# Kernel optimization log

Measured on AMD Instinct MI355X. Metric: run time of the kernel, lower is better.

## Reference

```python
import jax, jax.numpy as jnp
import numpy as np

T = 2048  # number of simulation steps


def setup_inputs() -> dict:
    key = jax.random.key(0)
    ks = jax.random.split(key, 7)
    B = 8192
    X = jax.random.uniform(ks[0], (T, B), dtype=jnp.float32)
    w_beta = jax.random.uniform(ks[1], (B,), dtype=jnp.float32)
    w_gamma = jax.random.uniform(ks[2], (B,), dtype=jnp.float32)
    w_sigma = jax.random.uniform(ks[3], (B,), dtype=jnp.float32)
    S0 = jax.random.uniform(ks[4], (B,), dtype=jnp.float32)
    I0 = jax.random.uniform(ks[5], (B,), dtype=jnp.float32)
    R0 = jax.random.uniform(ks[6], (B,), dtype=jnp.float32)
    N = jnp.ones((B,), dtype=jnp.float32)
    return {"X": X, "w_beta": w_beta, "w_gamma": w_gamma, "w_sigma": w_sigma,
            "S0": S0, "I0": I0, "R0": R0, "N": N}


def reference(X, w_beta, w_gamma, w_sigma, S0, I0, R0, N):
    # SEIR recurrence: state vectors of size B, scanned over T-1 steps.
    E0 = jnp.zeros_like(S0)

    def step(carry, x_t):
        S, E, I, R = carry
        beta = x_t * w_beta
        gamma = x_t * w_gamma
        sigma = x_t * w_sigma
        S_to_E = beta * I * S / N
        E_to_I = sigma * E
        I_to_R = gamma * I
        Sn = S - S_to_E
        En = E + S_to_E - E_to_I
        In = I + E_to_I - I_to_R
        Rn = R + I_to_R
        return (Sn, En, In, Rn), (Sn, En, In, Rn)

    # original loop runs t = 0 .. T-2, using X[t] at each step
    (_, _, _, _), (Ss, Es, Is, Rs) = jax.lax.scan(
        step, (S0, E0, I0, R0), X[: T - 1])

    S_ = jnp.concatenate([S0[None], Ss], axis=0)  # [T, B]
    E_ = jnp.concatenate([E0[None], Es], axis=0)
    I_ = jnp.concatenate([I0[None], Is], axis=0)
    R_ = jnp.concatenate([R0[None], Rs], axis=0)
    return S_, E_, I_, R_
```

## Files before the change

kernel.cpp:

```cpp
#include <hip/hip_runtime.h>

#define TSTEPS 2048
#define BCOLS  8192
#define TBSZ   (TSTEPS * BCOLS)
#define CHUNKS 32
#define CLEN   64

__device__ __forceinline__ void seir_step(float x, float wb, float wg, float wsg,
                                          float invN,
                                          float& S, float& E, float& I, float& R)
{
    const float s2e = x * wb * I * S * invN;
    const float e2i = x * wsg * E;
    const float i2r = x * wg * I;
    S = S - s2e;
    E = E + s2e - e2i;
    I = I + e2i - i2r;
    R = R + i2r;
}

__global__ __launch_bounds__(64)
void seir_pass1(const float* __restrict__ X,
                const float* __restrict__ w_beta,
                const float* __restrict__ w_gamma,
                const float* __restrict__ w_sigma,
                const float* __restrict__ S0,
                const float* __restrict__ I0,
                const float* __restrict__ R0,
                const float* __restrict__ Nv,
                float* __restrict__ wsp)
{
    const int b = blockIdx.x * 64 + threadIdx.x;

    const float wb  = w_beta[b];
    const float wg  = w_gamma[b];
    const float wsg = w_sigma[b];
    float S = S0[b];
    float E = 0.0f;
    float I = I0[b];
    float R = R0[b];
    const float invN = 1.0f / Nv[b];

    const float* xp = X + b;
    float xbuf[48];
#pragma unroll
    for (int k = 0; k < 48; ++k)
        xbuf[k] = xp[(size_t)k * BCOLS];
    xp += (size_t)48 * BCOLS;

    for (int j = 0; j < 41; ++j) {
        const int tbase = j * 48;
#pragma unroll
        for (int k = 0; k < 48; ++k) {
            const float x = xbuf[k];
            xbuf[k] = xp[(size_t)k * BCOLS];
            seir_step(x, wb, wg, wsg, invN, S, E, I, R);
            const int t = tbase + k;
            if (((t - 62) & 63) == 0) {
                const int idx = (t - 62) >> 6;
                float* wp = wsp + (size_t)idx * 4 * BCOLS + b;
                wp[0]                  = S;
                wp[(size_t)BCOLS]      = E;
                wp[(size_t)2 * BCOLS]  = I;
                wp[(size_t)3 * BCOLS]  = R;
            }
        }
        xp += (size_t)48 * BCOLS;
    }
#pragma unroll
    for (int k = 0; k < 15; ++k) {
        const float x = xbuf[k];
        seir_step(x, wb, wg, wsg, invN, S, E, I, R);
        if (((1968 + k - 62) & 63) == 0) {
            const int idx = (1968 + k - 62) >> 6;
            float* wp = wsp + (size_t)idx * 4 * BCOLS + b;
            wp[0]                  = S;
            wp[(size_t)BCOLS]      = E;
            wp[(size_t)2 * BCOLS]  = I;
            wp[(size_t)3 * BCOLS]  = R;
        }
    }
}

template <int NS>
__device__ __forceinline__ void run_chunk(const float* __restrict__ xp,
                                          float* __restrict__ pS,
                                          float* __restrict__ pE,
                                          float* __restrict__ pI,
                                          float* __restrict__ pR,
                                          float wb, float wg, float wsg, float invN,
                                          float S, float E, float I, float R)
{
    float xbuf[8];
#pragma unroll
    for (int k = 0; k < 8; ++k)
        xbuf[k] = xp[(size_t)k * BCOLS];
#pragma unroll
    for (int t = 0; t < NS; ++t) {
        const float x = xbuf[t & 7];
        if (t + 8 < NS)
            xbuf[t & 7] = xp[(size_t)(t + 8) * BCOLS];
        seir_step(x, wb, wg, wsg, invN, S, E, I, R);
        __builtin_nontemporal_store(S, pS + (size_t)t * BCOLS);
        __builtin_nontemporal_store(E, pE + (size_t)t * BCOLS);
        __builtin_nontemporal_store(I, pI + (size_t)t * BCOLS);
        __builtin_nontemporal_store(R, pR + (size_t)t * BCOLS);
    }
}

__global__ __launch_bounds__(64)
void seir_pass2(const float* __restrict__ X,
                const float* __restrict__ w_beta,
                const float* __restrict__ w_gamma,
                const float* __restrict__ w_sigma,
                const float* __restrict__ S0,
                const float* __restrict__ I0,
                const float* __restrict__ R0,
                const float* __restrict__ Nv,
                const float* __restrict__ wsp,
                float* __restrict__ out)
{
    const int b = blockIdx.x * 64 + threadIdx.x;
    const int c = blockIdx.y;

    const float wb  = w_beta[b];
    const float wg  = w_gamma[b];
    const float wsg = w_sigma[b];
    const float invN = 1.0f / Nv[b];

    float* oS = out + b;
    float* oE = out + (size_t)TBSZ + b;
    float* oI = out + (size_t)2 * TBSZ + b;
    float* oR = out + (size_t)3 * TBSZ + b;

    if (c == 0) {
        float S = S0[b];
        float E = 0.0f;
        float I = I0[b];
        float R = R0[b];
        __builtin_nontemporal_store(S, oS);
        __builtin_nontemporal_store(0.0f, oE);
        __builtin_nontemporal_store(I, oI);
        __builtin_nontemporal_store(R, oR);
        run_chunk<63>(X + b,
                      oS + BCOLS, oE + BCOLS, oI + BCOLS, oR + BCOLS,
                      wb, wg, wsg, invN, S, E, I, R);
    } else {
        const float* wp = wsp + (size_t)(c - 1) * 4 * BCOLS + b;
        const float S = wp[0];
        const float E = wp[(size_t)BCOLS];
        const float I = wp[(size_t)2 * BCOLS];
        const float R = wp[(size_t)3 * BCOLS];
        const size_t t0 = (size_t)c * CLEN - 1;
        const size_t r0 = (size_t)c * CLEN;
        run_chunk<64>(X + t0 * BCOLS + b,
                      oS + r0 * BCOLS, oE + r0 * BCOLS,
                      oI + r0 * BCOLS, oR + r0 * BCOLS,
                      wb, wg, wsg, invN, S, E, I, R);
    }
}

__global__ __launch_bounds__(64)
void seir_mono(const float* __restrict__ X,
               const float* __restrict__ w_beta,
               const float* __restrict__ w_gamma,
               const float* __restrict__ w_sigma,
               const float* __restrict__ S0,
               const float* __restrict__ I0,
               const float* __restrict__ R0,
               const float* __restrict__ Nv,
               float* __restrict__ out)
{
    const int b = blockIdx.x * 64 + threadIdx.x;
    const float wb  = w_beta[b];
    const float wg  = w_gamma[b];
    const float wsg = w_sigma[b];
    float S = S0[b];
    float E = 0.0f;
    float I = I0[b];
    float R = R0[b];
    const float invN = 1.0f / Nv[b];

    float* oS = out + b;
    float* oE = out + (size_t)TBSZ + b;
    float* oI = out + (size_t)2 * TBSZ + b;
    float* oR = out + (size_t)3 * TBSZ + b;

    __builtin_nontemporal_store(S, oS);
    __builtin_nontemporal_store(0.0f, oE);
    __builtin_nontemporal_store(I, oI);
    __builtin_nontemporal_store(R, oR);

    const float* xp = X + b;
    float xc[8];
#pragma unroll
    for (int k = 0; k < 8; ++k)
        xc[k] = __builtin_nontemporal_load(xp + (size_t)k * BCOLS);
    xp += (size_t)8 * BCOLS;

    for (int i = 0; i < 255; ++i) {
        float xn[8];
#pragma unroll
        for (int k = 0; k < 8; ++k)
            xn[k] = __builtin_nontemporal_load(xp + (size_t)k * BCOLS);
        xp += (size_t)8 * BCOLS;

        float* pS = oS + (size_t)(8 * i + 1) * BCOLS;
        float* pE = oE + (size_t)(8 * i + 1) * BCOLS;
        float* pI = oI + (size_t)(8 * i + 1) * BCOLS;
        float* pR = oR + (size_t)(8 * i + 1) * BCOLS;

#pragma unroll
        for (int k = 0; k < 8; ++k) {
            seir_step(xc[k], wb, wg, wsg, invN, S, E, I, R);
            __builtin_nontemporal_store(S, pS + (size_t)k * BCOLS);
            __builtin_nontemporal_store(E, pE + (size_t)k * BCOLS);
            __builtin_nontemporal_store(I, pI + (size_t)k * BCOLS);
            __builtin_nontemporal_store(R, pR + (size_t)k * BCOLS);
        }
#pragma unroll
        for (int k = 0; k < 8; ++k) xc[k] = xn[k];
    }
    {
        float* pS = oS + (size_t)2041 * BCOLS;
        float* pE = oE + (size_t)2041 * BCOLS;
        float* pI = oI + (size_t)2041 * BCOLS;
        float* pR = oR + (size_t)2041 * BCOLS;
#pragma unroll
        for (int k = 0; k < 7; ++k) {
            seir_step(xc[k], wb, wg, wsg, invN, S, E, I, R);
            __builtin_nontemporal_store(S, pS + (size_t)k * BCOLS);
            __builtin_nontemporal_store(E, pE + (size_t)k * BCOLS);
            __builtin_nontemporal_store(I, pI + (size_t)k * BCOLS);
            __builtin_nontemporal_store(R, pR + (size_t)k * BCOLS);
        }
    }
}

extern "C" void kernel_launch(void* const* d_in, const int* in_sizes, int n_in,
                              void* d_out, int out_size, void* d_ws, size_t ws_size,
                              hipStream_t stream)
{
    const float* X      = (const float*)d_in[0];
    const float* w_beta = (const float*)d_in[1];
    const float* w_gamma= (const float*)d_in[2];
    const float* w_sigma= (const float*)d_in[3];
    const float* S0     = (const float*)d_in[4];
    const float* I0     = (const float*)d_in[5];
    const float* R0     = (const float*)d_in[6];
    const float* Nv     = (const float*)d_in[7];
    float* out          = (float*)d_out;

    const size_t need = (size_t)(CHUNKS - 1) * 4 * BCOLS * sizeof(float);
    if (ws_size < need) {
        seir_mono<<<dim3(BCOLS / 64), dim3(64), 0, stream>>>(
            X, w_beta, w_gamma, w_sigma, S0, I0, R0, Nv, out);
        return;
    }

    float* wsp = (float*)d_ws;
    seir_pass1<<<dim3(BCOLS / 64), dim3(64), 0, stream>>>(
        X, w_beta, w_gamma, w_sigma, S0, I0, R0, Nv, wsp);
    seir_pass2<<<dim3(BCOLS / 64, CHUNKS), dim3(64), 0, stream>>>(
        X, w_beta, w_gamma, w_sigma, S0, I0, R0, Nv, wsp, out);
}
```

Before: 378.1 us.

## Fuse checkpoint and chunk-replay passes into one persistent kernel with flag handoff

Replaces the two-kernel scheme (a serial checkpoint pass, then a chunked replay that writes the output) with a single launch. Producer blocks run the full recurrence at raised priority and publish per-chunk state checkpoints with release flags. Consumer blocks spin on those flags and replay their chunks, so output writing overlaps the serial scan instead of waiting for it to finish. The change adds a memset, spin-waits that depend on producers and consumers being co-resident, and a timeout fallback that recomputes the prefix from scratch.

Result: slower. 1.315 ms (+247.7%).

```diff
diff --git a/kernel.cpp b/kernel.cpp
--- a/kernel.cpp
+++ b/kernel.cpp
@@ -5,6 +5,10 @@
 #define TBSZ   (TSTEPS * BCOLS)
 #define CHUNKS 32
 #define CLEN   64
+#define NGRP   128
+#define PBLK   32
+#define NCONS  512
+#define RING   32
 
 __device__ __forceinline__ void seir_step(float x, float wb, float wg, float wsg,
                                           float invN,
@@ -17,69 +21,6 @@
     E = E + s2e - e2i;
     I = I + e2i - i2r;
     R = R + i2r;
-}
-
-__global__ __launch_bounds__(64)
-void seir_pass1(const float* __restrict__ X,
-                const float* __restrict__ w_beta,
-                const float* __restrict__ w_gamma,
-                const float* __restrict__ w_sigma,
-                const float* __restrict__ S0,
-                const float* __restrict__ I0,
-                const float* __restrict__ R0,
-                const float* __restrict__ Nv,
-                float* __restrict__ wsp)
-{
-    const int b = blockIdx.x * 64 + threadIdx.x;
-
-    const float wb  = w_beta[b];
-    const float wg  = w_gamma[b];
-    const float wsg = w_sigma[b];
-    float S = S0[b];
-    float E = 0.0f;
-    float I = I0[b];
-    float R = R0[b];
-    const float invN = 1.0f / Nv[b];
-
-    const float* xp = X + b;
-    float xbuf[48];
-#pragma unroll
-    for (int k = 0; k < 48; ++k)
-        xbuf[k] = xp[(size_t)k * BCOLS];
-    xp += (size_t)48 * BCOLS;
-
-    for (int j = 0; j < 41; ++j) {
-        const int tbase = j * 48;
-#pragma unroll
-        for (int k = 0; k < 48; ++k) {
-            const float x = xbuf[k];
-            xbuf[k] = xp[(size_t)k * BCOLS];
-            seir_step(x, wb, wg, wsg, invN, S, E, I, R);
-            const int t = tbase + k;
-            if (((t - 62) & 63) == 0) {
-                const int idx = (t - 62) >> 6;
-                float* wp = wsp + (size_t)idx * 4 * BCOLS + b;
-                wp[0]                  = S;
-                wp[(size_t)BCOLS]      = E;
-                wp[(size_t)2 * BCOLS]  = I;
-                wp[(size_t)3 * BCOLS]  = R;
-            }
-        }
-        xp += (size_t)48 * BCOLS;
-    }
-#pragma unroll
-    for (int k = 0; k < 15; ++k) {
-        const float x = xbuf[k];
-        seir_step(x, wb, wg, wsg, invN, S, E, I, R);
-        if (((1968 + k - 62) & 63) == 0) {
-            const int idx = (1968 + k - 62) >> 6;
-            float* wp = wsp + (size_t)idx * 4 * BCOLS + b;
-            wp[0]                  = S;
-            wp[(size_t)BCOLS]      = E;
-            wp[(size_t)2 * BCOLS]  = I;
-            wp[(size_t)3 * BCOLS]  = R;
-        }
-    }
 }
 
 template <int NS>
@@ -108,26 +49,15 @@
     }
 }
 
-__global__ __launch_bounds__(64)
-void seir_pass2(const float* __restrict__ X,
-                const float* __restrict__ w_beta,
-                const float* __restrict__ w_gamma,
-                const float* __restrict__ w_sigma,
-                const float* __restrict__ S0,
-                const float* __restrict__ I0,
-                const float* __restrict__ R0,
-                const float* __restrict__ Nv,
-                const float* __restrict__ wsp,
-                float* __restrict__ out)
-{
-    const int b = blockIdx.x * 64 + threadIdx.x;
-    const int c = blockIdx.y;
-
-    const float wb  = w_beta[b];
-    const float wg  = w_gamma[b];
-    const float wsg = w_sigma[b];
-    const float invN = 1.0f / Nv[b];
-
+__device__ __forceinline__ void consume_chunk(
+    int c, int b, int g,
+    const float* __restrict__ X,
+    const float* __restrict__ S0, const float* __restrict__ I0,
+    const float* __restrict__ R0,
+    const float* __restrict__ wsp, const unsigned* __restrict__ flags,
+    float* __restrict__ out,
+    float wb, float wg, float wsg, float invN)
+{
     float* oS = out + b;
     float* oE = out + (size_t)TBSZ + b;
     float* oI = out + (size_t)2 * TBSZ + b;
@@ -145,18 +75,133 @@
         run_chunk<63>(X + b,
                       oS + BCOLS, oE + BCOLS, oI + BCOLS, oR + BCOLS,
                       wb, wg, wsg, invN, S, E, I, R);
+        return;
+    }
+
+    const unsigned* fp = &flags[(c - 1) * NGRP + g];
+    unsigned f;
+    int spins = 0;
+    while ((f = __hip_atomic_load(fp, __ATOMIC_ACQUIRE,
+                                  __HIP_MEMORY_SCOPE_AGENT)) == 0u) {
+        __builtin_amdgcn_s_sleep(8);
+        if (++spins > (1 << 20)) break;
+    }
+
+    float S, E, I, R;
+    if (f != 0u) {
+        const float* wp = wsp + (size_t)(c - 1) * 4 * BCOLS + b;
+        S = wp[0];
+        E = wp[(size_t)BCOLS];
+        I = wp[(size_t)2 * BCOLS];
+        R = wp[(size_t)3 * BCOLS];
     } else {
-        const float* wp = wsp + (size_t)(c - 1) * 4 * BCOLS + b;
-        const float S = wp[0];
-        const float E = wp[(size_t)BCOLS];
-        const float I = wp[(size_t)2 * BCOLS];
-        const float R = wp[(size_t)3 * BCOLS];
-        const size_t t0 = (size_t)c * CLEN - 1;
-        const size_t r0 = (size_t)c * CLEN;
-        run_chunk<64>(X + t0 * BCOLS + b,
-                      oS + r0 * BCOLS, oE + r0 * BCOLS,
-                      oI + r0 * BCOLS, oR + r0 * BCOLS,
-                      wb, wg, wsg, invN, S, E, I, R);
+        S = S0[b];
+        E = 0.0f;
+        I = I0[b];
+        R = R0[b];
+        const float* xq = X + b;
+        const int nst = 64 * c - 1;
+#pragma unroll 4
+        for (int t = 0; t < nst; ++t)
+            seir_step(xq[(size_t)t * BCOLS], wb, wg, wsg, invN, S, E, I, R);
+    }
+
+    const size_t t0 = (size_t)c * CLEN - 1;
+    const size_t r0 = (size_t)c * CLEN;
+    run_chunk<64>(X + t0 * BCOLS + b,
+                  oS + r0 * BCOLS, oE + r0 * BCOLS,
+                  oI + r0 * BCOLS, oR + r0 * BCOLS,
+                  wb, wg, wsg, invN, S, E, I, R);
+}
+
+__global__ __launch_bounds__(256, 4)
+void seir_fused(const float* __restrict__ X,
+                const float* __restrict__ w_beta,
+                const float* __restrict__ w_gamma,
+                const float* __restrict__ w_sigma,
+                const float* __restrict__ S0,
+                const float* __restrict__ I0,
+                const float* __restrict__ R0,
+                const float* __restrict__ Nv,
+                float* __restrict__ wsp,
+                unsigned* __restrict__ flags,
+                float* __restrict__ out)
+{
+    const int wave = threadIdx.x >> 6;
+    const int lane = threadIdx.x & 63;
+
+    if (blockIdx.x < PBLK) {
+        const int g = blockIdx.x * 4 + wave;
+        const int b = g * 64 + lane;
+
+        __builtin_amdgcn_s_setprio(1);
+
+        const float wb  = w_beta[b];
+        const float wg  = w_gamma[b];
+        const float wsg = w_sigma[b];
+        const float invN = 1.0f / Nv[b];
+        float S = S0[b];
+        float E = 0.0f;
+        float I = I0[b];
+        float R = R0[b];
+
+        const float* xp = X + b;
+        float ring[RING];
+#pragma unroll
+        for (int k = 0; k < RING; ++k)
+            ring[k] = xp[(size_t)k * BCOLS];
+        xp += (size_t)RING * BCOLS;
+
+        for (int j = 0; j < 61; ++j) {
+#pragma unroll
+            for (int k = 0; k < RING; ++k) {
+                const float x = ring[k];
+                ring[k] = xp[(size_t)k * BCOLS];
+                seir_step(x, wb, wg, wsg, invN, S, E, I, R);
+                if (k == 30 && (j & 1)) {
+                    const int idx = (j - 1) >> 1;
+                    float* wp = wsp + (size_t)idx * 4 * BCOLS + b;
+                    wp[0]                 = S;
+                    wp[(size_t)BCOLS]     = E;
+                    wp[(size_t)2 * BCOLS] = I;
+                    wp[(size_t)3 * BCOLS] = R;
+                    if (lane == 0)
+                        __hip_atomic_store(&flags[idx * NGRP + g], 1u,
+                                           __ATOMIC_RELEASE,
+                                           __HIP_MEMORY_SCOPE_AGENT);
+                }
+            }
+            xp += (size_t)RING * BCOLS;
+        }
+#pragma unroll
+        for (int k = 0; k < 31; ++k)
+            seir_step(ring[k], wb, wg, wsg, invN, S, E, I, R);
+        {
+            float* wp = wsp + (size_t)30 * 4 * BCOLS + b;
+            wp[0]                 = S;
+            wp[(size_t)BCOLS]     = E;
+            wp[(size_t)2 * BCOLS] = I;
+            wp[(size_t)3 * BCOLS] = R;
+            if (lane == 0)
+                __hip_atomic_store(&flags[30 * NGRP + g], 1u,
+                                   __ATOMIC_RELEASE, __HIP_MEMORY_SCOPE_AGENT);
+        }
+    } else {
+        const int idx = (int)blockIdx.x - PBLK;
+        const int G   = idx & 31;
+        const int cp  = idx >> 5;
+        const int g   = G * 4 + wave;
+        const int b   = g * 64 + lane;
+
+        const float wb  = w_beta[b];
+        const float wg  = w_gamma[b];
+        const float wsg = w_sigma[b];
+        const float invN = 1.0f / Nv[b];
+
+        consume_chunk(cp, b, g, X, S0, I0, R0, wsp, flags, out,
+                      wb, wg, wsg, invN);
+        consume_chunk(cp + 16, b, g, X, S0, I0, R0, wsp, flags, out,
+                      wb, wg, wsg, invN);
     }
 }
 
@@ -241,6 +286,8 @@
                               void* d_out, int out_size, void* d_ws, size_t ws_size,
                               hipStream_t stream)
 {
+    (void)in_sizes; (void)n_in; (void)out_size;
+
     const float* X      = (const float*)d_in[0];
     const float* w_beta = (const float*)d_in[1];
     const float* w_gamma= (const float*)d_in[2];
@@ -251,16 +298,19 @@
     const float* Nv     = (const float*)d_in[7];
     float* out          = (float*)d_out;
 
-    const size_t need = (size_t)(CHUNKS - 1) * 4 * BCOLS * sizeof(float);
-    if (ws_size < need) {
+    const size_t state_bytes = (size_t)(CHUNKS - 1) * 4 * BCOLS * sizeof(float);
+    const size_t flag_bytes  = (size_t)(CHUNKS - 1) * NGRP * sizeof(unsigned);
+    if (ws_size < state_bytes + flag_bytes) {
         seir_mono<<<dim3(BCOLS / 64), dim3(64), 0, stream>>>(
             X, w_beta, w_gamma, w_sigma, S0, I0, R0, Nv, out);
         return;
     }
 
-    float* wsp = (float*)d_ws;
-    seir_pass1<<<dim3(BCOLS / 64), dim3(64), 0, stream>>>(
-        X, w_beta, w_gamma, w_sigma, S0, I0, R0, Nv, wsp);
-    seir_pass2<<<dim3(BCOLS / 64, CHUNKS), dim3(64), 0, stream>>>(
-        X, w_beta, w_gamma, w_sigma, S0, I0, R0, Nv, wsp, out);
-}
+    float* wsp      = (float*)d_ws;
+    unsigned* flags = (unsigned*)((char*)d_ws + state_bytes);
+
+    hipMemsetAsync(flags, 0, flag_bytes, stream);
+
+    seir_fused<<<dim3(PBLK + NCONS), dim3(256), 0, stream>>>(
+        X, w_beta, w_gamma, w_sigma, S0, I0, R0, Nv, wsp, flags, out);
+}
```

## Vectorize pass2 to four columns per thread and restructure pass1 prefetch ring

Applied to the files above, without the earlier changes.

Pass2 now has each thread handle four adjacent columns using float4 loads and float4 nontemporal stores, which cuts its grid by four and issues wider memory transactions. Pass1 drops its 48-deep array buffer for 32 named registers in a 32-step unrolled loop, writing checkpoints at fixed positions with no per-step index test. Both kernels get launch_bounds(64,1). The trade-off is fewer waves in pass2 (1024 blocks of 64), so less latency hiding, and higher register pressure.

New measurement: 405.2 us. 7.2% more time.

```diff
diff --git a/kernel.cpp b/kernel.cpp
--- a/kernel.cpp
+++ b/kernel.cpp
@@ -5,6 +5,8 @@
 #define TBSZ   (TSTEPS * BCOLS)
 #define CHUNKS 32
 #define CLEN   64
+
+typedef float f4 __attribute__((ext_vector_type(4)));
 
 __device__ __forceinline__ void seir_step(float x, float wb, float wg, float wsg,
                                           float invN,
@@ -19,7 +21,18 @@
     R = R + i2r;
 }
 
-__global__ __launch_bounds__(64)
+__device__ __forceinline__ void seir_step4(f4 x, f4 wb, f4 wg, f4 wsg, f4 iN,
+                                           f4& S, f4& E, f4& I, f4& R)
+{
+#pragma unroll
+    for (int c = 0; c < 4; ++c) {
+        float s = S[c], e = E[c], i = I[c], r = R[c];
+        seir_step(x[c], wb[c], wg[c], wsg[c], iN[c], s, e, i, r);
+        S[c] = s; E[c] = e; I[c] = i; R[c] = r;
+    }
+}
+
+__global__ __launch_bounds__(64, 1)
 void seir_pass1(const float* __restrict__ X,
                 const float* __restrict__ w_beta,
                 const float* __restrict__ w_gamma,
@@ -35,80 +48,101 @@
     const float wb  = w_beta[b];
     const float wg  = w_gamma[b];
     const float wsg = w_sigma[b];
+    const float invN = 1.0f / Nv[b];
     float S = S0[b];
     float E = 0.0f;
     float I = I0[b];
     float R = R0[b];
-    const float invN = 1.0f / Nv[b];
 
     const float* xp = X + b;
-    float xbuf[48];
-#pragma unroll
-    for (int k = 0; k < 48; ++k)
-        xbuf[k] = xp[(size_t)k * BCOLS];
-    xp += (size_t)48 * BCOLS;
-
-    for (int j = 0; j < 41; ++j) {
-        const int tbase = j * 48;
-#pragma unroll
-        for (int k = 0; k < 48; ++k) {
-            const float x = xbuf[k];
-            xbuf[k] = xp[(size_t)k * BCOLS];
-            seir_step(x, wb, wg, wsg, invN, S, E, I, R);
-            const int t = tbase + k;
-            if (((t - 62) & 63) == 0) {
-                const int idx = (t - 62) >> 6;
-                float* wp = wsp + (size_t)idx * 4 * BCOLS + b;
-                wp[0]                  = S;
-                wp[(size_t)BCOLS]      = E;
-                wp[(size_t)2 * BCOLS]  = I;
-                wp[(size_t)3 * BCOLS]  = R;
-            }
+
+#define PRELOAD(i) float r##i = xp[(size_t)(i) * BCOLS];
+    PRELOAD(0)  PRELOAD(1)  PRELOAD(2)  PRELOAD(3)
+    PRELOAD(4)  PRELOAD(5)  PRELOAD(6)  PRELOAD(7)
+    PRELOAD(8)  PRELOAD(9)  PRELOAD(10) PRELOAD(11)
+    PRELOAD(12) PRELOAD(13) PRELOAD(14) PRELOAD(15)
+    PRELOAD(16) PRELOAD(17) PRELOAD(18) PRELOAD(19)
+    PRELOAD(20) PRELOAD(21) PRELOAD(22) PRELOAD(23)
+    PRELOAD(24) PRELOAD(25) PRELOAD(26) PRELOAD(27)
+    PRELOAD(28) PRELOAD(29) PRELOAD(30) PRELOAD(31)
+#undef PRELOAD
+    xp += (size_t)32 * BCOLS;
+
+#define PSTEP(i) do {                                                   \
+        const float x_ = r##i;                                          \
+        r##i = xp[(size_t)(i) * BCOLS];                                 \
+        seir_step(x_, wb, wg, wsg, invN, S, E, I, R);                   \
+    } while (0)
+
+    for (int j = 0; j < 61; ++j) {
+        PSTEP(0);  PSTEP(1);  PSTEP(2);  PSTEP(3);
+        PSTEP(4);  PSTEP(5);  PSTEP(6);  PSTEP(7);
+        PSTEP(8);  PSTEP(9);  PSTEP(10); PSTEP(11);
+        PSTEP(12); PSTEP(13); PSTEP(14); PSTEP(15);
+        PSTEP(16); PSTEP(17); PSTEP(18); PSTEP(19);
+        PSTEP(20); PSTEP(21); PSTEP(22); PSTEP(23);
+        PSTEP(24); PSTEP(25); PSTEP(26); PSTEP(27);
+        PSTEP(28); PSTEP(29);
+        PSTEP(30);
+        if (j & 1) {
+            const int idx = (j - 1) >> 1;
+            float* wp = wsp + (size_t)idx * 4 * BCOLS + b;
+            wp[0]                 = S;
+            wp[(size_t)BCOLS]     = E;
+            wp[(size_t)2 * BCOLS] = I;
+            wp[(size_t)3 * BCOLS] = R;
         }
-        xp += (size_t)48 * BCOLS;
-    }
-#pragma unroll
-    for (int k = 0; k < 15; ++k) {
-        const float x = xbuf[k];
-        seir_step(x, wb, wg, wsg, invN, S, E, I, R);
-        if (((1968 + k - 62) & 63) == 0) {
-            const int idx = (1968 + k - 62) >> 6;
-            float* wp = wsp + (size_t)idx * 4 * BCOLS + b;
-            wp[0]                  = S;
-            wp[(size_t)BCOLS]      = E;
-            wp[(size_t)2 * BCOLS]  = I;
-            wp[(size_t)3 * BCOLS]  = R;
-        }
+        PSTEP(31);
+        xp += (size_t)32 * BCOLS;
+    }
+#undef PSTEP
+
+#define DSTEP(i) seir_step(r##i, wb, wg, wsg, invN, S, E, I, R);
+    DSTEP(0)  DSTEP(1)  DSTEP(2)  DSTEP(3)
+    DSTEP(4)  DSTEP(5)  DSTEP(6)  DSTEP(7)
+    DSTEP(8)  DSTEP(9)  DSTEP(10) DSTEP(11)
+    DSTEP(12) DSTEP(13) DSTEP(14) DSTEP(15)
+    DSTEP(16) DSTEP(17) DSTEP(18) DSTEP(19)
+    DSTEP(20) DSTEP(21) DSTEP(22) DSTEP(23)
+    DSTEP(24) DSTEP(25) DSTEP(26) DSTEP(27)
+    DSTEP(28) DSTEP(29) DSTEP(30)
+#undef DSTEP
+    {
+        float* wp = wsp + (size_t)30 * 4 * BCOLS + b;
+        wp[0]                 = S;
+        wp[(size_t)BCOLS]     = E;
+        wp[(size_t)2 * BCOLS] = I;
+        wp[(size_t)3 * BCOLS] = R;
     }
 }
 
 template <int NS>
-__device__ __forceinline__ void run_chunk(const float* __restrict__ xp,
-                                          float* __restrict__ pS,
-                                          float* __restrict__ pE,
-                                          float* __restrict__ pI,
-                                          float* __restrict__ pR,
-                                          float wb, float wg, float wsg, float invN,
-                                          float S, float E, float I, float R)
-{
-    float xbuf[8];
+__device__ __forceinline__ void run_chunk4(const float* __restrict__ xp,
+                                           float* __restrict__ pS,
+                                           float* __restrict__ pE,
+                                           float* __restrict__ pI,
+                                           float* __restrict__ pR,
+                                           f4 wb, f4 wg, f4 wsg, f4 iN,
+                                           f4 S, f4 E, f4 I, f4 R)
+{
+    f4 xbuf[8];
 #pragma unroll
     for (int k = 0; k < 8; ++k)
-        xbuf[k] = xp[(size_t)k * BCOLS];
+        xbuf[k] = *(const f4*)(xp + (size_t)k * BCOLS);
 #pragma unroll
     for (int t = 0; t < NS; ++t) {
-        const float x = xbuf[t & 7];
+        const f4 x = xbuf[t & 7];
         if (t + 8 < NS)
-            xbuf[t & 7] = xp[(size_t)(t + 8) * BCOLS];
-        seir_step(x, wb, wg, wsg, invN, S, E, I, R);
-        __builtin_nontemporal_store(S, pS + (size_t)t * BCOLS);
-        __builtin_nontemporal_store(E, pE + (size_t)t * BCOLS);
-        __builtin_nontemporal_store(I, pI + (size_t)t * BCOLS);
-        __builtin_nontemporal_store(R, pR + (size_t)t * BCOLS);
-    }
-}
-
-__global__ __launch_bounds__(64)
+            xbuf[t & 7] = *(const f4*)(xp + (size_t)(t + 8) * BCOLS);
+        seir_step4(x, wb, wg, wsg, iN, S, E, I, R);
+        __builtin_nontemporal_store(S, (f4*)(pS + (size_t)t * BCOLS));
+        __builtin_nontemporal_store(E, (f4*)(pE + (size_t)t * BCOLS));
+        __builtin_nontemporal_store(I, (f4*)(pI + (size_t)t * BCOLS));
+        __builtin_nontemporal_store(R, (f4*)(pR + (size_t)t * BCOLS));
+    }
+}
+
+__global__ __launch_bounds__(64, 1)
 void seir_pass2(const float* __restrict__ X,
                 const float* __restrict__ w_beta,
                 const float* __restrict__ w_gamma,
@@ -120,43 +154,47 @@
                 const float* __restrict__ wsp,
                 float* __restrict__ out)
 {
-    const int b = blockIdx.x * 64 + threadIdx.x;
-    const int c = blockIdx.y;
-
-    const float wb  = w_beta[b];
-    const float wg  = w_gamma[b];
-    const float wsg = w_sigma[b];
-    const float invN = 1.0f / Nv[b];
-
-    float* oS = out + b;
-    float* oE = out + (size_t)TBSZ + b;
-    float* oI = out + (size_t)2 * TBSZ + b;
-    float* oR = out + (size_t)3 * TBSZ + b;
+    const int tid = blockIdx.x * 64 + threadIdx.x;
+    const int cb  = tid * 4;
+    const int c   = blockIdx.y;
+
+    const f4 wb  = *(const f4*)(w_beta  + cb);
+    const f4 wg  = *(const f4*)(w_gamma + cb);
+    const f4 wsg = *(const f4*)(w_sigma + cb);
+    const f4 n4  = *(const f4*)(Nv + cb);
+    f4 iN;
+#pragma unroll
+    for (int k = 0; k < 4; ++k) iN[k] = 1.0f / n4[k];
+
+    float* oS = out + cb;
+    float* oE = out + (size_t)TBSZ + cb;
+    float* oI = out + (size_t)2 * TBSZ + cb;
+    float* oR = out + (size_t)3 * TBSZ + cb;
 
     if (c == 0) {
-        float S = S0[b];
-        float E = 0.0f;
-        float I = I0[b];
-        float R = R0[b];
-        __builtin_nontemporal_store(S, oS);
-        __builtin_nontemporal_store(0.0f, oE);
-        __builtin_nontemporal_store(I, oI);
-        __builtin_nontemporal_store(R, oR);
-        run_chunk<63>(X + b,
-                      oS + BCOLS, oE + BCOLS, oI + BCOLS, oR + BCOLS,
-                      wb, wg, wsg, invN, S, E, I, R);
+        const f4 S = *(const f4*)(S0 + cb);
+        const f4 E = {0.0f, 0.0f, 0.0f, 0.0f};
+        const f4 I = *(const f4*)(I0 + cb);
+        const f4 R = *(const f4*)(R0 + cb);
+        __builtin_nontemporal_store(S, (f4*)oS);
+        __builtin_nontemporal_store(E, (f4*)oE);
+        __builtin_nontemporal_store(I, (f4*)oI);
+        __builtin_nontemporal_store(R, (f4*)oR);
+        run_chunk4<63>(X + cb,
+                       oS + BCOLS, oE + BCOLS, oI + BCOLS, oR + BCOLS,
+                       wb, wg, wsg, iN, S, E, I, R);
     } else {
-        const float* wp = wsp + (size_t)(c - 1) * 4 * BCOLS + b;
-        const float S = wp[0];
-        const float E = wp[(size_t)BCOLS];
-        const float I = wp[(size_t)2 * BCOLS];
-        const float R = wp[(size_t)3 * BCOLS];
+        const float* wp = wsp + (size_t)(c - 1) * 4 * BCOLS + cb;
+        const f4 S = *(const f4*)(wp);
+        const f4 E = *(const f4*)(wp + (size_t)BCOLS);
+        const f4 I = *(const f4*)(wp + (size_t)2 * BCOLS);
+        const f4 R = *(const f4*)(wp + (size_t)3 * BCOLS);
         const size_t t0 = (size_t)c * CLEN - 1;
         const size_t r0 = (size_t)c * CLEN;
-        run_chunk<64>(X + t0 * BCOLS + b,
-                      oS + r0 * BCOLS, oE + r0 * BCOLS,
-                      oI + r0 * BCOLS, oR + r0 * BCOLS,
-                      wb, wg, wsg, invN, S, E, I, R);
+        run_chunk4<64>(X + t0 * BCOLS + cb,
+                       oS + r0 * BCOLS, oE + r0 * BCOLS,
+                       oI + r0 * BCOLS, oR + r0 * BCOLS,
+                       wb, wg, wsg, iN, S, E, I, R);
     }
 }
 
@@ -241,6 +279,8 @@
                               void* d_out, int out_size, void* d_ws, size_t ws_size,
                               hipStream_t stream)
 {
+    (void)in_sizes; (void)n_in; (void)out_size;
+
     const float* X      = (const float*)d_in[0];
     const float* w_beta = (const float*)d_in[1];
     const float* w_gamma= (const float*)d_in[2];
@@ -261,6 +301,6 @@
     float* wsp = (float*)d_ws;
     seir_pass1<<<dim3(BCOLS / 64), dim3(64), 0, stream>>>(
         X, w_beta, w_gamma, w_sigma, S0, I0, R0, Nv, wsp);
-    seir_pass2<<<dim3(BCOLS / 64, CHUNKS), dim3(64), 0, stream>>>(
+    seir_pass2<<<dim3(BCOLS / 256, CHUNKS), dim3(64), 0, stream>>>(
         X, w_beta, w_gamma, w_sigma, S0, I0, R0, Nv, wsp, out);
 }
```
